# Performance work log

Measured on AMD Instinct MI355X. Metric: run time of the kernel, lower is better.

Reference implementation:

```python
import jax, jax.numpy as jnp
import numpy as np

# ---- grid / frustum config (from default grid_config & data_config) ----
DB = (1.0, 60.0, 1.0)                 # dbound
OGH, OGW, DS = 256, 704, 16           # input size, downsample
FH, FW = OGH // DS, OGW // DS         # 16, 44
DEPTH = int(round((DB[1] - DB[0]) / DB[2]))  # 59 depth bins
NX0, NX1, NZ = 128, 128, 1            # BEV grid
DX = np.array([0.8, 0.8, 20.0], np.float32)
BX = np.array([-51.2 + 0.4, -51.2 + 0.4, 0.0], np.float32)  # row0 + dx/2


def _frustum():
    # (D, FH, FW, 3): pixel (u, v, depth)
    ds = jnp.broadcast_to(jnp.arange(DB[0], DB[1], DB[2], dtype=jnp.float32).reshape(-1, 1, 1), (DEPTH, FH, FW))
    xs = jnp.broadcast_to(jnp.linspace(0.0, OGW - 1.0, FW, dtype=jnp.float32).reshape(1, 1, FW), (DEPTH, FH, FW))
    ys = jnp.broadcast_to(jnp.linspace(0.0, OGH - 1.0, FH, dtype=jnp.float32).reshape(1, FH, 1), (DEPTH, FH, FW))
    return jnp.stack([xs, ys, ds], axis=-1)


def _geometry(rots, trans, intrins, post_rots, post_trans, bda):
    # pixel frustum -> ego-frame 3D points; (B, N, D, FH, FW, 3)
    pts = _frustum() - post_trans[:, :, None, None, None, :]
    pts = jnp.einsum('bnij,bndhwj->bndhwi', jnp.linalg.inv(post_rots), pts)
    pts = jnp.concatenate([pts[..., :2] * pts[..., 2:3], pts[..., 2:3]], axis=-1)
    comb = jnp.einsum('bnij,bnjk->bnik', rots, jnp.linalg.inv(intrins))
    pts = jnp.einsum('bnij,bndhwj->bndhwi', comb, pts) + trans[:, :, None, None, None, :]
    pts = jnp.einsum('bij,bndhwj->bndhwi', bda, pts)
    return pts


def _voxel_pool(geom, vol):
    # geom: (B,N,D,FH,FW,3), vol: (B,N,D,FH,FW,C) -> BEV (B, C*NZ, NX0, NX1)
    B, C = vol.shape[0], vol.shape[-1]
    gidx = jnp.floor((geom - (BX - DX / 2.0)) / DX).astype(jnp.int32)
    kept = ((gidx[..., 0] >= 0) & (gidx[..., 0] < NX0)
            & (gidx[..., 1] >= 0) & (gidx[..., 1] < NX1)
            & (gidx[..., 2] >= 0) & (gidx[..., 2] < NZ))
    bidx = jnp.broadcast_to(jnp.arange(B, dtype=jnp.int32).reshape(B, 1, 1, 1, 1), gidx.shape[:-1])
    flat = ((bidx * NZ + gidx[..., 2]) * NX0 + gidx[..., 0]) * NX1 + gidx[..., 1]
    nvox = B * NZ * NX0 * NX1
    flat = jnp.where(kept, flat, nvox).reshape(-1)      # dump bucket for culled pts
    feats = vol.reshape(-1, C)
    bev = jax.ops.segment_sum(feats, flat, num_segments=nvox + 1)[:nvox]
    bev = bev.reshape(B, NZ, NX0, NX1, C)
    bev = jnp.moveaxis(bev, -1, 2).reshape(B, NZ * C, NX0, NX1)  # z-major channel cat
    return bev


def setup_inputs() -> dict:
    key = jax.random.key(0)
    B, N, CIN, CT = 4, 6, 512, 64
    k1, k2 = jax.random.split(key, 2)
    x = jax.random.normal(k1, (B, N, CIN, FH, FW), dtype=jnp.float32)
    weight = jax.random.normal(k2, (DEPTH + CT, CIN), dtype=jnp.float32) * 0.02
    bias = jnp.zeros((DEPTH + CT,), dtype=jnp.float32)
    # cam->ego rotation (cam z forward -> ego x, cam x right -> ego -y, cam y down -> ego -z)
    Rcam = jnp.asarray(np.array([[0., 0., 1.], [-1., 0., 0.], [0., -1., 0.]], np.float32))
    rots = jnp.tile(Rcam, (B, N, 1, 1))
    trans = jnp.zeros((B, N, 3), dtype=jnp.float32)
    K = jnp.asarray(np.array([[600., 0., 352.], [0., 600., 128.], [0., 0., 1.]], np.float32))
    intrins = jnp.tile(K, (B, N, 1, 1))
    post_rots = jnp.tile(jnp.eye(3, dtype=jnp.float32), (B, N, 1, 1))
    post_trans = jnp.zeros((B, N, 3), dtype=jnp.float32)
    bda = jnp.tile(jnp.eye(3, dtype=jnp.float32), (B, 1, 1))
    return dict(x=x, rots=rots, trans=trans, intrins=intrins, post_rots=post_rots,
                post_trans=post_trans, bda=bda, weight=weight, bias=bias)


def reference(x, rots, trans, intrins, post_rots, post_trans, bda, weight, bias):
    # 1x1 depth/context head (eval mode): (B,N,Cin,H,W) -> (B,N,D+C,H,W)
    out = jnp.einsum('bnchw,oc->bnohw', x, weight) + bias[None, None, :, None, None]
    depth = jax.nn.softmax(out[:, :, :DEPTH], axis=2)      # (B,N,D,H,W)
    feat = out[:, :, DEPTH:]                               # (B,N,C,H,W)
    # depth-context outer product -> frustum volume (B,N,D,H,W,C)
    vol = jnp.einsum('bndhw,bnchw->bndhwc', depth, feat)
    geom = _geometry(rots, trans, intrins, post_rots, post_trans, bda)
    bev = _voxel_pool(geom, vol)                           # (B, C*NZ, 128, 128)
    return bev, depth
```

## Files before the change

### kernel.cpp

```cpp
#include <hip/hip_runtime.h>
#include <math.h>

#define CIN   512
#define NOUT  123
#define DEPN  59
#define CT    64
#define B_    4
#define N_    6
#define FH    16
#define FW    44
#define HW    704
#define NPIX  (B_*N_*HW)
#define NX    128
#define BEV_ELEMS (B_*CT*NX*NX)
#define DEPTH_OFF BEV_ELEMS

#define WS_WB   1920
#define WS_PS   (WS_WB + 32768)
#define WS_FS   (WS_PS + NPIX*64)
#define WS_GC   (WS_FS + NPIX*64)

typedef short bf16x8 __attribute__((ext_vector_type(8)));
typedef float f32x4  __attribute__((ext_vector_type(4)));

__device__ inline unsigned short f2bf(float f) {
    unsigned u = __float_as_uint(f);
    return (unsigned short)((u + 0x7fffu + ((u >> 16) & 1u)) >> 16);
}

__device__ inline void inv3d(const double* m, double* o) {
    #pragma clang fp contract(off)
    double c00 = m[4]*m[8] - m[5]*m[7];
    double c01 = m[5]*m[6] - m[3]*m[8];
    double c02 = m[3]*m[7] - m[4]*m[6];
    double det = m[0]*c00 + m[1]*c01 + m[2]*c02;
    o[0] = c00/det; o[1] = (m[2]*m[7]-m[1]*m[8])/det; o[2] = (m[1]*m[5]-m[2]*m[4])/det;
    o[3] = c01/det; o[4] = (m[0]*m[8]-m[2]*m[6])/det; o[5] = (m[2]*m[3]-m[0]*m[5])/det;
    o[6] = c02/det; o[7] = (m[1]*m[6]-m[0]*m[7])/det; o[8] = (m[0]*m[4]-m[1]*m[3])/det;
}
__device__ inline void mm3d(const double* a, const double* b, double* o) {
    #pragma clang fp contract(off)
    for (int i = 0; i < 3; ++i)
        for (int k = 0; k < 3; ++k)
            o[i*3+k] = (a[i*3+0]*b[0*3+k] + a[i*3+1]*b[1*3+k]) + a[i*3+2]*b[2*3+k];
}

__global__ __launch_bounds__(256) void k0_prep(
        const float* __restrict__ rots,  const float* __restrict__ trans,
        const float* __restrict__ intr,  const float* __restrict__ prots,
        const float* __restrict__ ptrans,const float* __restrict__ bda,
        const float* __restrict__ W,     float* __restrict__ ws,
        float* __restrict__ dout) {
    __shared__ double sTd[24][33];
    const int tid = threadIdx.x;
    const int bid = blockIdx.x;
    int gtid = bid * 256 + tid;
    int stride = gridDim.x * 256;
    float4 z = {0.f, 0.f, 0.f, 0.f};
    for (int i = gtid; i < BEV_ELEMS / 4; i += stride)
        *(float4*)(dout + 4 * (size_t)i) = z;
    unsigned short* wb = (unsigned short*)(ws + WS_WB);
    for (int i = gtid; i < 128 * CIN; i += stride) {
        int o = i >> 9, c = i & 511;
        wb[i] = (o < NOUT) ? f2bf(W[o * CIN + c]) : (unsigned short)0;
    }
    if (bid >= 66) return;
    if (tid < B_ * N_) {
        #pragma clang fp contract(off)
        int t = tid, b = t / N_;
        double* X = sTd[t];
        double PR[9], Kd[9], Rd[9], Bd[9];
        for (int i = 0; i < 9; ++i) PR[i] = (double)prots[t * 9 + i];
        for (int i = 0; i < 9; ++i) Kd[i] = (double)intr[t * 9 + i];
        for (int i = 0; i < 9; ++i) Rd[i] = (double)rots[t * 9 + i];
        for (int i = 0; i < 9; ++i) Bd[i] = (double)bda[b * 9 + i];
        double iPR[9]; inv3d(PR, iPR);
        for (int i = 0; i < 9; ++i) X[i] = iPR[i];
        for (int i = 0; i < 3; ++i) X[9 + i] = (double)ptrans[t * 3 + i];
        double iK[9];  inv3d(Kd, iK);
        double comb[9]; mm3d(Rd, iK, comb);
        for (int i = 0; i < 9; ++i) X[12 + i] = comb[i];
        for (int i = 0; i < 3; ++i) X[21 + i] = (double)trans[t * 3 + i];
        for (int i = 0; i < 9; ++i) X[24 + i] = Bd[i];
    }
    __syncthreads();
    {
        #pragma clang fp contract(off)
        int i = bid * 256 + tid;
        int b = i / (FW * 96);
        int rem = i - b * (FW * 96);
        int w = rem / 96;
        int j = rem - w * 96;
        int n = j >> 4, h = j & 15;
        const double* T = sTd[b * N_ + n];
        const double xs = (w == 43) ? 703.0 : (double)w * (703.0 / 43.0);
        const double ys = (double)(h * 17);
        const double u0 = xs - T[9];
        const double u1 = ys - T[10];
        double pA[3], pB[3];
        #pragma unroll
        for (int k = 0; k < 3; ++k) {
            pA[k] = (T[3*k]*u0 + T[3*k+1]*u1) - T[3*k+2]*T[11];
            pB[k] = T[3*k+2];
        }
        double q0c[3] = { pA[0]*pA[2], pA[0]*pB[2] + pB[0]*pA[2], pB[0]*pB[2] };
        double q1c[3] = { pA[1]*pA[2], pA[1]*pB[2] + pB[1]*pA[2], pB[1]*pB[2] };
        double q2c[3] = { pA[2], pB[2], 0.0 };
        double rc[3][3], gc[3][3];
        #pragma unroll
        for (int r = 0; r < 3; ++r)
            #pragma unroll
            for (int k = 0; k < 3; ++k)
                rc[r][k] = ((T[12+3*r]*q0c[k] + T[13+3*r]*q1c[k]) + T[14+3*r]*q2c[k])
                           + ((k == 0) ? T[21+r] : 0.0);
        #pragma unroll
        for (int g = 0; g < 3; ++g)
            #pragma unroll
            for (int k = 0; k < 3; ++k)
                gc[g][k] = (T[24+3*g]*rc[0][k] + T[25+3*g]*rc[1][k]) + T[26+3*g]*rc[2][k];
        double* dst = (double*)(ws) + WS_GC / 2 + (size_t)i * 9;
        #pragma unroll
        for (int q = 0; q < 9; ++q) dst[q] = gc[q / 3][q % 3];
    }
}

#define K1A   4608
#define K1T   13824
__global__ __launch_bounds__(256, 2) void k1_gemm(const float* __restrict__ x,
                                                  const float* __restrict__ bias,
                                                  float* __restrict__ ws,
                                                  float* __restrict__ dout) {
    __shared__ __align__(16) unsigned short s16[2 * K1T];
    const int tid = threadIdx.x;
    const int wave = tid >> 6, lane = tid & 63;
    const int l15 = lane & 15, quad = lane >> 4;
    const int bn = blockIdx.y;
    const int pixbase = blockIdx.x * 64;
    const float* xg = x + (size_t)bn * CIN * HW + pixbase;
    const unsigned short* wbg = (const unsigned short*)(ws + WS_WB);
    const int cpack = tid >> 4;
    const int pix4 = (tid & 15) * 4;
    const int wo  = tid >> 3;
    const int wsub = tid & 7;

    f32x4 acc[8] = {};
    float4 xr0, xr1, xr2, xr3;
    uint4  wr4[4];
    {
        const float* src = xg + (size_t)(4 * cpack) * HW + pix4;
        xr0 = *(const float4*)(src);
        xr1 = *(const float4*)(src + HW);
        xr2 = *(const float4*)(src + 2 * HW);
        xr3 = *(const float4*)(src + 3 * HW);
        #pragma unroll
        for (int i = 0; i < 4; ++i)
            wr4[i] = *(const uint4*)(wbg + (size_t)(wo + 32 * i) * CIN + wsub * 8);
    }
    #pragma unroll
    for (int it = 0; it < 8; ++it) {
        const int buf = it & 1;
        unsigned short* sa = s16 + buf * K1T;
        unsigned short* sb = sa + K1A;
        {
            const float* f0 = (const float*)&xr0; const float* f1 = (const float*)&xr1;
            const float* f2 = (const float*)&xr2; const float* f3 = (const float*)&xr3;
            #pragma unroll
            for (int i = 0; i < 4; ++i) {
                uint2 pk;
                pk.x = (unsigned)f2bf(f0[i]) | ((unsigned)f2bf(f1[i]) << 16);
                pk.y = (unsigned)f2bf(f2[i]) | ((unsigned)f2bf(f3[i]) << 16);
                *(uint2*)&sa[(pix4 + i) * 72 + 4 * cpack] = pk;
            }
            #pragma unroll
            for (int i = 0; i < 4; ++i)
                *(uint4*)&sb[(wo + 32 * i) * 72 + wsub * 8] = wr4[i];
        }
        if (it < 7) {
            const int ck = (it + 1) * 64;
            const float* src = xg + (size_t)(ck + 4 * cpack) * HW + pix4;
            xr0 = *(const float4*)(src);
            xr1 = *(const float4*)(src + HW);
            xr2 = *(const float4*)(src + 2 * HW);
            xr3 = *(const float4*)(src + 3 * HW);
            #pragma unroll
            for (int i = 0; i < 4; ++i)
                wr4[i] = *(const uint4*)(wbg + (size_t)(wo + 32 * i) * CIN + ck + wsub * 8);
        }
        __syncthreads();
        #pragma unroll
        for (int ks = 0; ks < 64; ks += 32) {
            const bf16x8 a = *(const bf16x8*)&sa[(wave * 16 + l15) * 72 + ks + quad * 8];
            #pragma unroll
            for (int nt = 0; nt < 8; ++nt) {
                const bf16x8 b = *(const bf16x8*)&sb[(nt * 16 + l15) * 72 + ks + quad * 8];
                acc[nt] = __builtin_amdgcn_mfma_f32_16x16x32_bf16(a, b, acc[nt], 0, 0, 0);
            }
        }
    }
    float* sred = (float*)s16;
    const int b = bn / N_, n = bn - b * N_;
    {
        float bb[8];
        #pragma unroll
        for (int nt = 0; nt < 8; ++nt) {
            int o = nt * 16 + l15;
            bb[nt] = (o < NOUT) ? bias[o] : 0.0f;
        }
        float* ps = ws + WS_PS;
        float* fs = ws + WS_FS;
        #pragma unroll
        for (int reg = 0; reg < 4; ++reg) {
            int pixl = wave * 16 + quad * 4 + reg;
            int pix = pixbase + pixl;
            int h = pix / FW, w = pix - h * FW;
            size_t row = (size_t)(b * FW + w) * 96 + n * FH + h;
            float v[4]; float m = -INFINITY;
            #pragma unroll
            for (int nt = 0; nt < 4; ++nt) {
                v[nt] = acc[nt][reg] + bb[nt];
                if (nt * 16 + l15 < DEPN) m = fmaxf(m, v[nt]);
            }
            #pragma unroll
            for (int msk = 8; msk >= 1; msk >>= 1) m = fmaxf(m, __shfl_xor(m, msk, 64));
            float e[4], s = 0.0f;
            #pragma unroll
            for (int nt = 0; nt < 4; ++nt) {
                e[nt] = (nt * 16 + l15 < DEPN) ? expf(v[nt] - m) : 0.0f;
                s += e[nt];
            }
            #pragma unroll
            for (int msk = 8; msk >= 1; msk >>= 1) s += __shfl_xor(s, msk, 64);
            const float inv = 1.0f / s;
            #pragma unroll
            for (int nt = 0; nt < 4; ++nt) {
                int o = nt * 16 + l15;
                if (o < DEPN) {
                    float p = e[nt] * inv;
                    ps[row * 64 + o] = p;
                    sred[pixl * 65 + o] = p;
                } else fs[row * 64 + (o - DEPN)] = v[nt];
            }
            #pragma unroll
            for (int nt = 4; nt < 8; ++nt) {
                int o = nt * 16 + l15;
                if (o < NOUT) fs[row * 64 + (o - DEPN)] = acc[nt][reg] + bb[nt];
            }
        }
    }
    __syncthreads();
    for (int o = wave; o < DEPN; o += 4)
        dout[DEPTH_OFF + ((size_t)bn * DEPN + o) * HW + pixbase + lane] = sred[lane * 65 + o];
}

#define DQ2 16
__global__ __launch_bounds__(256) void k2b_geom(float* __restrict__ ws,
                                                float* __restrict__ dout) {
    __shared__ float sF[96][64];
    __shared__ float sP[DQ2][100];
    __shared__ unsigned short sv16[DQ2 * 96];
    __shared__ __align__(16) double sG[96 * 9];
    __shared__ int sflag[DQ2];
    const int tid = threadIdx.x;
    const int bw = blockIdx.x;
    const int b = bw / FW;
    const int dbase = blockIdx.y * DQ2;
    const int nd = min(DQ2, DEPN - dbase);

    {
        const float* fsrc = ws + WS_FS + (size_t)bw * (96 * 64);
        const float* psrc = ws + WS_PS + (size_t)bw * (96 * 64);
        for (int i = tid; i < 96 * 16; i += 256) {
            int j = i >> 4, c4 = (i & 15) * 4;
            *(float4*)&sF[j][c4] = *(const float4*)(fsrc + j * 64 + c4);
        }
        for (int i = tid; i < 96 * 4; i += 256) {
            int j = i >> 2, q = i & 3;
            const float4 p4 = *(const float4*)(psrc + j * 64 + dbase + 4 * q);
            sP[4 * q + 0][j] = p4.x; sP[4 * q + 1][j] = p4.y;
            sP[4 * q + 2][j] = p4.z; sP[4 * q + 3][j] = p4.w;
        }
        const double2* gsrc = (const double2*)((const double*)(ws) + WS_GC / 2
                                               + (size_t)bw * (96 * 9));
        for (int i = tid; i < 432; i += 256)
            ((double2*)sG)[i] = gsrc[i];
    }
    __syncthreads();

    {
        const double BXY = (double)(-51.2000007629394531f);
        for (int idx = tid; idx < nd * 96; idx += 256) {
            int dl = idx / 96, j = idx - dl * 96;
            const double* G = &sG[j * 9];
            const double dsv = (double)(dbase + dl + 1);
            const double g0 = (G[2] * dsv + G[1]) * dsv + G[0];
            const double g1 = (G[5] * dsv + G[4]) * dsv + G[3];
            const double g2 = (G[8] * dsv + G[7]) * dsv + G[6];
            const double fx = floor((g0 - BXY) * 1.25);
            const double fy = floor((g1 - BXY) * 1.25);
            const bool keep = (fx >= 0.0) & (fx < 128.0) & (fy >= 0.0) & (fy < 128.0) &
                              (g2 >= -10.0) & (g2 < 10.0);
            sv16[idx] = keep ? (unsigned short)((int)fx * NX + (int)fy)
                             : (unsigned short)0xFFFF;
        }
    }
    __syncthreads();

    {
        const int dl = tid >> 4, s = tid & 15;
        int u = -1, mix = 0;
        const int base = dl * 96 + s * 6;
        #pragma unroll
        for (int t = 0; t < 6; ++t) {
            int v = sv16[base + t];
            if (v != 0xFFFF) { if (u < 0) u = v; else if (v != u) mix = 1; }
        }
        #pragma unroll
        for (int msk = 1; msk < 16; msk <<= 1) {
            int uo = __shfl_xor(u, msk, 64);
            int mo = __shfl_xor(mix, msk, 64);
            mix = mix | mo | ((u >= 0 && uo >= 0 && uo != u) ? 1 : 0);
            u = (u < 0) ? uo : u;
        }
        if (s == 0 && dl < nd) sflag[dl] = mix ? -2 : u;
    }
    for (int idx = tid; idx < nd * 96; idx += 256) {
        if (sv16[idx] == 0xFFFF) {
            int dl = idx / 96, j = idx - dl * 96;
            sP[dl][j] = 0.0f;
        }
    }
    __syncthreads();

    const int dl = tid >> 4, ci = tid & 15;
    if (dl < nd && sflag[dl] >= 0) {
        float ax = 0.f, ay = 0.f, az = 0.f, aw = 0.f;
        for (int jj = 0; jj < 96; jj += 4) {
            const float4 pv = *(const float4*)&sP[dl][jj];
            const float4 f0 = *(const float4*)&sF[jj + 0][4 * ci];
            const float4 f1 = *(const float4*)&sF[jj + 1][4 * ci];
            const float4 f2 = *(const float4*)&sF[jj + 2][4 * ci];
            const float4 f3 = *(const float4*)&sF[jj + 3][4 * ci];
            ax = fmaf(pv.x, f0.x, ax); ay = fmaf(pv.x, f0.y, ay);
            az = fmaf(pv.x, f0.z, az); aw = fmaf(pv.x, f0.w, aw);
            ax = fmaf(pv.y, f1.x, ax); ay = fmaf(pv.y, f1.y, ay);
            az = fmaf(pv.y, f1.z, az); aw = fmaf(pv.y, f1.w, aw);
            ax = fmaf(pv.z, f2.x, ax); ay = fmaf(pv.z, f2.y, ay);
            az = fmaf(pv.z, f2.z, az); aw = fmaf(pv.z, f2.w, aw);
            ax = fmaf(pv.w, f3.x, ax); ay = fmaf(pv.w, f3.y, ay);
            az = fmaf(pv.w, f3.z, az); aw = fmaf(pv.w, f3.w, aw);
        }
        float* dst = dout + (((size_t)(b * CT + 4 * ci)) << 14) + sflag[dl];
        atomicAdd(dst,             ax);
        atomicAdd(dst + (1 << 14), ay);
        atomicAdd(dst + (2 << 14), az);
        atomicAdd(dst + (3 << 14), aw);
    }
    for (int d2 = 0; d2 < nd; ++d2) {
        if (sflag[d2] == -2) {
            int c = tid & 63, g = tid >> 6;
            for (int jj = 0; jj < 24; ++jj) {
                int j = g * 24 + jj;
                int v = sv16[d2 * 96 + j];
                if (v != 0xFFFF)
                    atomicAdd(dout + (((size_t)(b * CT + c)) << 14) + v,
                              sP[d2][j] * sF[j][c]);
            }
        }
    }
}

extern "C" void kernel_launch(void* const* d_in, const int* in_sizes, int n_in,
                              void* d_out, int out_size, void* d_ws, size_t ws_size,
                              hipStream_t stream) {
    const float* x      = (const float*)d_in[0];
    const float* rots   = (const float*)d_in[1];
    const float* trans  = (const float*)d_in[2];
    const float* intr   = (const float*)d_in[3];
    const float* prots  = (const float*)d_in[4];
    const float* ptrans = (const float*)d_in[5];
    const float* bda    = (const float*)d_in[6];
    const float* W      = (const float*)d_in[7];
    const float* bias   = (const float*)d_in[8];
    float* out = (float*)d_out;
    float* ws  = (float*)d_ws;

    k0_prep<<<512, 256, 0, stream>>>(rots, trans, intr, prots, ptrans, bda, W, ws, out);
    k1_gemm<<<dim3(HW / 64, B_ * N_), 256, 0, stream>>>(x, bias, ws, out);
    k2b_geom<<<dim3(B_ * FW, 4), 256, 0, stream>>>(ws, out);
}
```

Measured before the change: 157.5 us.

## Replace global atomic BEV scatter with staged per-chunk shared-memory accumulation kernel

```diff
diff --git a/kernel.cpp b/kernel.cpp
--- a/kernel.cpp
+++ b/kernel.cpp
@@ -19,6 +19,8 @@
 #define WS_PS   (WS_WB + 32768)
 #define WS_FS   (WS_PS + NPIX*64)
 #define WS_GC   (WS_FS + NPIX*64)
+#define WS_C    (WS_GC + NPIX*18)
+#define WS_VOX  (WS_C + B_*FW*DEPN*64)
 
 typedef short bf16x8 __attribute__((ext_vector_type(8)));
 typedef float f32x4  __attribute__((ext_vector_type(4)));
@@ -332,28 +334,30 @@
     __syncthreads();
 
     const int dl = tid >> 4, ci = tid & 15;
-    if (dl < nd && sflag[dl] >= 0) {
-        float ax = 0.f, ay = 0.f, az = 0.f, aw = 0.f;
-        for (int jj = 0; jj < 96; jj += 4) {
-            const float4 pv = *(const float4*)&sP[dl][jj];
-            const float4 f0 = *(const float4*)&sF[jj + 0][4 * ci];
-            const float4 f1 = *(const float4*)&sF[jj + 1][4 * ci];
-            const float4 f2 = *(const float4*)&sF[jj + 2][4 * ci];
-            const float4 f3 = *(const float4*)&sF[jj + 3][4 * ci];
-            ax = fmaf(pv.x, f0.x, ax); ay = fmaf(pv.x, f0.y, ay);
-            az = fmaf(pv.x, f0.z, az); aw = fmaf(pv.x, f0.w, aw);
-            ax = fmaf(pv.y, f1.x, ax); ay = fmaf(pv.y, f1.y, ay);
-            az = fmaf(pv.y, f1.z, az); aw = fmaf(pv.y, f1.w, aw);
-            ax = fmaf(pv.z, f2.x, ax); ay = fmaf(pv.z, f2.y, ay);
-            az = fmaf(pv.z, f2.z, az); aw = fmaf(pv.z, f2.w, aw);
-            ax = fmaf(pv.w, f3.x, ax); ay = fmaf(pv.w, f3.y, ay);
-            az = fmaf(pv.w, f3.z, az); aw = fmaf(pv.w, f3.w, aw);
-        }
-        float* dst = dout + (((size_t)(b * CT + 4 * ci)) << 14) + sflag[dl];
-        atomicAdd(dst,             ax);
-        atomicAdd(dst + (1 << 14), ay);
-        atomicAdd(dst + (2 << 14), az);
-        atomicAdd(dst + (3 << 14), aw);
+    if (dl < nd) {
+        const int flag = sflag[dl];
+        if (ci == 0)
+            ((int*)(ws + WS_VOX))[bw * DEPN + dbase + dl] = (flag >= 0) ? flag : -1;
+        if (flag >= 0) {
+            float ax = 0.f, ay = 0.f, az = 0.f, aw = 0.f;
+            for (int jj = 0; jj < 96; jj += 4) {
+                const float4 pv = *(const float4*)&sP[dl][jj];
+                const float4 f0 = *(const float4*)&sF[jj + 0][4 * ci];
+                const float4 f1 = *(const float4*)&sF[jj + 1][4 * ci];
+                const float4 f2 = *(const float4*)&sF[jj + 2][4 * ci];
+                const float4 f3 = *(const float4*)&sF[jj + 3][4 * ci];
+                ax = fmaf(pv.x, f0.x, ax); ay = fmaf(pv.x, f0.y, ay);
+                az = fmaf(pv.x, f0.z, az); aw = fmaf(pv.x, f0.w, aw);
+                ax = fmaf(pv.y, f1.x, ax); ay = fmaf(pv.y, f1.y, ay);
+                az = fmaf(pv.y, f1.z, az); aw = fmaf(pv.y, f1.w, aw);
+                ax = fmaf(pv.z, f2.x, ax); ay = fmaf(pv.z, f2.y, ay);
+                az = fmaf(pv.z, f2.z, az); aw = fmaf(pv.z, f2.w, aw);
+                ax = fmaf(pv.w, f3.x, ax); ay = fmaf(pv.w, f3.y, ay);
+                az = fmaf(pv.w, f3.z, az); aw = fmaf(pv.w, f3.w, aw);
+            }
+            float4 st = { ax, ay, az, aw };
+            *(float4*)&ws[WS_C + ((size_t)(bw * DEPN + dbase + dl)) * 64 + 4 * ci] = st;
+        }
     }
     for (int d2 = 0; d2 < nd; ++d2) {
         if (sflag[d2] == -2) {
@@ -366,6 +370,49 @@
                               sP[d2][j] * sF[j][c]);
             }
         }
+    }
+}
+
+#define CHUNK 128
+__global__ __launch_bounds__(256) void k2c_scatter(const float* __restrict__ ws,
+                                                   float* __restrict__ dout) {
+    __shared__ float acc[64][CHUNK + 4];
+    __shared__ int   sVox[FW * DEPN];
+    __shared__ short sMatch[FW * DEPN];
+    __shared__ int   nMatch;
+    const int tid = threadIdx.x;
+    const int base = blockIdx.x * CHUNK;
+    const int b = blockIdx.y;
+    for (int i = tid; i < 64 * (CHUNK + 4); i += 256) (&acc[0][0])[i] = 0.0f;
+    if (tid == 0) nMatch = 0;
+    const int* vsrc = (const int*)(ws + WS_VOX) + b * (FW * DEPN);
+    for (int i = tid; i < FW * DEPN; i += 256) sVox[i] = vsrc[i];
+    __syncthreads();
+    for (int i = tid; i < FW * DEPN; i += 256) {
+        int v = sVox[i];
+        if ((unsigned)(v - base) < CHUNK) {
+            int m = atomicAdd(&nMatch, 1);
+            sMatch[m] = (short)i;
+        }
+    }
+    __syncthreads();
+    const int c = tid & 63, quarter = tid >> 6;
+    const int nm = nMatch;
+    for (int m = quarter; m < nm; m += 4) {
+        int e = sMatch[m];
+        int lv = sVox[e] - base;
+        float val = ws[WS_C + ((size_t)b * (FW * DEPN) + e) * 64 + c];
+        atomicAdd(&acc[c][lv], val);
+    }
+    __syncthreads();
+    const int wave = tid >> 6, lane = tid & 63;
+    float* outb = dout + (((size_t)(b * CT)) << 14) + base;
+    for (int r = wave; r < 64; r += 4) {
+        float2* dst = (float2*)(outb + ((size_t)r << 14) + lane * 2);
+        float2 v = *dst;
+        v.x += acc[r][lane * 2];
+        v.y += acc[r][lane * 2 + 1];
+        *dst = v;
     }
 }
 
@@ -387,4 +434,5 @@
     k0_prep<<<512, 256, 0, stream>>>(rots, trans, intr, prots, ptrans, bda, W, ws, out);
     k1_gemm<<<dim3(HW / 64, B_ * N_), 256, 0, stream>>>(x, bias, ws, out);
     k2b_geom<<<dim3(B_ * FW, 4), 256, 0, stream>>>(ws, out);
-}
+    k2c_scatter<<<dim3(NX * NX / CHUNK, B_), 256, 0, stream>>>(ws, out);
+}
```

After: 150.4 us. -4.5%, faster.
